# Optimization experiments

Hardware: AMD Instinct MI355X
Metric: run time of the kernel (lower is better)

Reference implementation:

```python
import jax, jax.numpy as jnp
import numpy as np
from jax import lax

HEADS = 8
C, H, W = 64, 16, 16
D_K = C // HEADS
SCALE = 1.0 / np.sqrt(D_K * H * W).astype(np.float32)


def conv2d(x, w, b):
    # x: [N, C, H, W], w: [O, I, 3, 3], padding=1
    y = lax.conv_general_dilated(x, w, window_strides=(1, 1),
                                 padding=((1, 1), (1, 1)),
                                 dimension_numbers=('NCHW', 'OIHW', 'NCHW'))
    return y + b[None, :, None, None]


def _project(x, w, b, bs, seq):
    # x: [bs, seq, C, H, W] -> conv per frame -> [bs, heads, seq, d_k*H*W]
    y = conv2d(x.reshape(bs * seq, C, H, W), w, b)
    y = y.reshape(bs, seq, HEADS, D_K, H, W)
    y = jnp.transpose(y, (0, 2, 1, 3, 4, 5)).reshape(bs, HEADS, seq, D_K * H * W)
    return y


def setup_inputs() -> dict:
    key = jax.random.key(0)
    ks = jax.random.split(key, 11)
    shp = (2, 256, C, H, W)
    wstd = 1.0 / np.sqrt(C * 9)  # torch Conv2d default init scale
    inp = {
        'q': jax.random.normal(ks[0], shp, jnp.float32),
        'k': jax.random.normal(ks[1], shp, jnp.float32),
        'v': jax.random.normal(ks[2], shp, jnp.float32),
        'Wq': jax.random.uniform(ks[3], (C, C, 3, 3), jnp.float32, -wstd, wstd),
        'bq': jax.random.uniform(ks[4], (C,), jnp.float32, -wstd, wstd),
        'Wk': jax.random.uniform(ks[5], (C, C, 3, 3), jnp.float32, -wstd, wstd),
        'bk': jax.random.uniform(ks[6], (C,), jnp.float32, -wstd, wstd),
        'Wv': jax.random.uniform(ks[7], (C, C, 3, 3), jnp.float32, -wstd, wstd),
        'bv': jax.random.uniform(ks[8], (C,), jnp.float32, -wstd, wstd),
        'Wo': jax.random.uniform(ks[9], (C, C, 3, 3), jnp.float32, -wstd, wstd),
        'bo': jax.random.uniform(ks[10], (C,), jnp.float32, -wstd, wstd),
    }
    return inp


def reference(q, k, v, Wq, bq, Wk, bk, Wv, bv, Wo, bo):
    bs, seq = q.shape[0], q.shape[1]
    qh = _project(q, Wq, bq, bs, seq)  # [bs, h, seq, d_k*H*W]
    kh = _project(k, Wk, bk, bs, seq)
    vh = _project(v, Wv, bv, bs, seq)
    scores = jnp.einsum('bhqd,bhkd->bhqk', qh, kh) * SCALE
    attn = jax.nn.softmax(scores, axis=-1)
    out = jnp.einsum('bhqk,bhkd->bhqd', attn, vh)  # [bs, h, seq, d_k*H*W]
    out = out.reshape(bs, HEADS, seq, D_K, H, W)
    concat = jnp.transpose(out, (0, 2, 1, 3, 4, 5)).reshape(bs * seq, C, H, W)
    y = conv2d(concat, Wo, bo).reshape(bs, seq, C, H, W)
    return y
```

## Files before the change

kernel.cpp:

```cpp
#include <hip/hip_runtime.h>
#include <hip/hip_bf16.h>
#include <hip/hip_fp16.h>

typedef unsigned short u16;
typedef _Float16 f16x8 __attribute__((ext_vector_type(8)));
typedef u16 u16x8 __attribute__((ext_vector_type(8)));
typedef u16 u16x4 __attribute__((ext_vector_type(4)));
typedef float f32x4 __attribute__((ext_vector_type(4)));

__device__ __forceinline__ u16 f2h(float f){
  __half h = __float2half(f);
  return *(u16*)&h;
}

__device__ __forceinline__ void cp16_async(const u16* g, u16* l){
  __builtin_amdgcn_global_load_lds(
      (const __attribute__((address_space(1))) unsigned int*)g,
      (__attribute__((address_space(3))) unsigned int*)l,
      16, 0, 0);
}

__device__ __forceinline__ void prep_w_body(const float* W, u16* Wt, int i){
  if (i >= 36864) return;
  int co = i / 576, rem = i % 576, ci = rem / 9, tap = rem % 9;
  int n = co >> 4, lr = co & 15, kk = ci >> 5, lg = (ci >> 3) & 3, j = ci & 7;
  int s = tap*2 + kk;
  Wt[(((s*4 + n)*64) + lg*16 + lr)*8 + j] = f2h(W[i]);
}

__global__ __launch_bounds__(256) void prep_w3(
    const float* __restrict__ Wq, const float* __restrict__ Wk,
    const float* __restrict__ Wv, u16* __restrict__ Wt)
{
  int which = blockIdx.y;
  const float* W = (which == 0) ? Wq : (which == 1) ? Wk : Wv;
  prep_w_body(W, Wt + which*36864, blockIdx.x * 256 + threadIdx.x);
}

__global__ __launch_bounds__(256) void prep_w(
    const float* __restrict__ W, u16* __restrict__ Wt)
{
  prep_w_body(W, Wt, blockIdx.x * 256 + threadIdx.x);
}

template<bool IN_F32, bool OUT_PROJ>
__device__ __forceinline__ void conv_body(
    const void* __restrict__ xin, const u16* __restrict__ Wt,
    const float* __restrict__ bias, void* __restrict__ dst,
    int frame, u16* xT, float* stage, int tid)
{
  #define STAGE_Q(qi, buf) do {                                             \
    if (IN_F32){                                                            \
      const float* src_ = (const float*)xin + (size_t)frame*16384 + (qi)*4096; \
      _Pragma("unroll")                                                     \
      for (int t_ = 0; t_ < 4; ++t_){                                       \
        int c_ = tid + t_*256;                                              \
        cp16_async((const u16*)(src_ + c_*4), (u16*)((float*)(buf) + c_*4));\
      }                                                                     \
    } else {                                                                \
      const u16* src_ = (const u16*)xin + (size_t)frame*16384 + (qi)*4096;  \
      _Pragma("unroll")                                                     \
      for (int t_ = 0; t_ < 2; ++t_){                                       \
        int c_ = tid + t_*256;                                              \
        cp16_async(src_ + c_*8, (u16*)(buf) + c_*8);                        \
      }                                                                     \
    }                                                                       \
  } while(0)

  float* S0 = stage;
  float* S1 = stage + 4096;

  STAGE_Q(0, S0);
  for (int i = tid; i < 2592; i += 256)
    *(uint4*)((char*)xT + i*16) = make_uint4(0u, 0u, 0u, 0u);
  __syncthreads();

  const int p = tid, py = p >> 4, px = p & 15;
  const int pp = (py + 1)*18 + px + 1;

  #pragma unroll 1
  for (int qi = 0; qi < 4; ++qi){
    if (qi < 3) STAGE_Q(qi + 1, (qi & 1) ? S0 : S1);
    const float* Sf = (qi & 1) ? S1 : S0;
    const u16*   Su = (const u16*)Sf;
    #pragma unroll
    for (int b = 0; b < 2; ++b){
      u16x8 pk;
      #pragma unroll
      for (int j = 0; j < 8; ++j)
        pk[j] = IN_F32 ? f2h(Sf[(b*8 + j)*256 + p]) : Su[(b*8 + j)*256 + p];
      unsigned cb = (unsigned)(qi*2 + b);
      unsigned off = (unsigned)(pp*128) + (((cb + (unsigned)pp) & 7u) << 4);
      *(u16x8*)((char*)xT + off) = pk;
    }
    __syncthreads();
  }

  const int w = tid >> 6, lane = tid & 63, lr = lane & 15, lg = lane >> 4;
  const int pyb = w * 4;

  f32x4 acc[4][4];
  #pragma unroll
  for (int n = 0; n < 4; ++n){
    float b = bias[n*16 + lr];
    #pragma unroll
    for (int m = 0; m < 4; ++m){
      acc[m][n][0] = b; acc[m][n][1] = b; acc[m][n][2] = b; acc[m][n][3] = b;
    }
  }

  #define LOADB(s, B) do {                                                  \
    _Pragma("unroll")                                                       \
    for (int n_ = 0; n_ < 4; ++n_)                                          \
      B[n_] = *(const f16x8*)(Wt + ((((s)*4 + n_)*64) + lane)*8);           \
  } while(0)

  #define STEP(s, B) do {                                                   \
    int tap_ = (s) >> 1, kk_ = (s) & 1;                                     \
    int dy_ = tap_ / 3, dx_ = tap_ - dy_*3;                                 \
    f16x8 af_[4];                                                           \
    _Pragma("unroll")                                                       \
    for (int m_ = 0; m_ < 4; ++m_){                                         \
      int pp_ = (pyb + m_ + dy_)*18 + lr + dx_;                             \
      unsigned slot_ = ((unsigned)(kk_*4 + lg) + (unsigned)pp_) & 7u;       \
      af_[m_] = *(const f16x8*)((const char*)xT                             \
                 + (unsigned)(pp_*128) + (slot_ << 4));                     \
    }                                                                       \
    _Pragma("unroll")                                                       \
    for (int m_ = 0; m_ < 4; ++m_)                                          \
      _Pragma("unroll")                                                     \
      for (int n_ = 0; n_ < 4; ++n_)                                        \
        acc[m_][n_] = __builtin_amdgcn_mfma_f32_16x16x32_f16(               \
            af_[m_], B[n_], acc[m_][n_], 0, 0, 0);                          \
  } while(0)

  f16x8 Ba[4], Bb[4];
  LOADB(0, Ba);
  #pragma unroll 1
  for (int it = 0; it < 9; ++it){
    LOADB(it*2 + 1, Bb);
    STEP(it*2, Ba);
    if (it < 8) LOADB(it*2 + 2, Ba);
    STEP(it*2 + 1, Bb);
  }
  #undef LOADB
  #undef STEP
  #undef STAGE_Q

  __syncthreads();
  char* xTc = (char*)xT;
  if (OUT_PROJ){
    #pragma unroll
    for (int n = 0; n < 4; ++n){
      int co = n*16 + lr;
      #pragma unroll
      for (int m = 0; m < 4; ++m){
        int px0 = w*64 + m*16 + lg*4;
        int s = px0 >> 3;
        unsigned aw = (unsigned)(co*512) + (unsigned)((s ^ (co & 7)) << 4)
                      + (unsigned)((px0 & 7) * 2);
        u16x4 o4;
        #pragma unroll
        for (int r = 0; r < 4; ++r) o4[r] = f2h(acc[m][n][r]);
        *(u16x4*)(xTc + aw) = o4;
      }
    }
    __syncthreads();
    u16* d = (u16*)dst;
    const int b = frame >> 8, sq = frame & 255;
    #pragma unroll
    for (int i = 0; i < 8; ++i){
      int c = w*8 + i;
      int co = c*2 + (lane >> 5);
      int pxo = (lane & 31) * 8;
      unsigned ld = (unsigned)(co*512) + (unsigned)(((lane & 31) ^ (co & 7)) << 4);
      uint4 v = *(const uint4*)(xTc + ld);
      int h = co >> 3, dk = co & 7;
      u16* gp = d + ((size_t)((b*8 + h)*256 + sq))*2048 + dk*256 + pxo;
      *(uint4*)gp = v;
    }
  } else {
    float* dfr = (float*)dst + (size_t)frame * 16384;
    #pragma unroll
    for (int ph2 = 0; ph2 < 2; ++ph2){
      if ((w >> 1) == ph2){
        #pragma unroll
        for (int n = 0; n < 4; ++n){
          int co = n*16 + lr;
          #pragma unroll
          for (int m = 0; m < 4; ++m){
            int pxl = (w & 1)*64 + m*16 + lg*4;
            int s = pxl >> 2;
            unsigned aw = (unsigned)(co*512) + (unsigned)((s ^ (co & 7)) << 4);
            *(f32x4*)(xTc + aw) = acc[m][n];
          }
        }
      }
      __syncthreads();
      #pragma unroll
      for (int i = 0; i < 8; ++i){
        int c = w*8 + i;
        int co = c*2 + (lane >> 5);
        int pxl = (lane & 31) * 4;
        unsigned ld = (unsigned)(co*512) + (unsigned)(((lane & 31) ^ (co & 7)) << 4);
        f32x4 v = *(const f32x4*)(xTc + ld);
        *(f32x4*)(dfr + co*256 + ph2*128 + pxl) = v;
      }
      if (ph2 == 0) __syncthreads();
    }
  }
}

__global__ __launch_bounds__(256, 2) void conv3_mfma(
    const float* __restrict__ q, const float* __restrict__ k,
    const float* __restrict__ v, const u16* __restrict__ Wt3,
    const float* __restrict__ bq, const float* __restrict__ bk,
    const float* __restrict__ bv,
    u16* __restrict__ qh, u16* __restrict__ kh, u16* __restrict__ vh)
{
  __shared__ __align__(16) u16 xT[324 * 64];
  __shared__ __align__(16) float stage[2*4096];
  const int which = blockIdx.x >> 9;
  const int frame = blockIdx.x & 511;
  const float* x = (which == 0) ? q : (which == 1) ? k : v;
  const float* bias = (which == 0) ? bq : (which == 1) ? bk : bv;
  u16* dst = (which == 0) ? qh : (which == 1) ? kh : vh;
  conv_body<true, true>(x, Wt3 + which*36864, bias, dst, frame, xT, stage, threadIdx.x);
}

__global__ __launch_bounds__(256, 2) void conv_out_mfma(
    const u16* __restrict__ xin, const u16* __restrict__ Wt,
    const float* __restrict__ bias, float* __restrict__ out)
{
  __shared__ __align__(16) u16 xT[324 * 64];
  __shared__ __align__(16) float stage[2*4096];
  conv_body<false, false>(xin, Wt, bias, out, blockIdx.x, xT, stage, threadIdx.x);
}

__global__ __launch_bounds__(256) void transpose_v(
    const u16* __restrict__ vh, u16* __restrict__ vt)
{
  __shared__ u16 tile[64][72];
  const int tid = threadIdx.x;
  const int dt = blockIdx.x, st = blockIdx.y, bh = blockIdx.z;
  {
    int r = tid >> 2, c4 = tid & 3;
    const u16* src = vh + ((size_t)(bh*256 + st*64 + r))*2048 + dt*64 + c4*16;
    uint4 v0 = *(const uint4*)src;
    uint4 v1 = *(const uint4*)(src + 8);
    *(uint4*)&tile[r][c4*16]     = v0;
    *(uint4*)&tile[r][c4*16 + 8] = v1;
  }
  __syncthreads();
  {
    int dr = tid >> 2, s4 = tid & 3;
    u16 tmp[16];
    #pragma unroll
    for (int i = 0; i < 16; ++i) tmp[i] = tile[s4*16 + i][dr];
    u16* dstp = vt + ((size_t)(bh*2048 + dt*64 + dr))*256 + st*64 + s4*16;
    *(uint4*)dstp       = *(uint4*)&tmp[0];
    *(uint4*)(dstp + 8) = *(uint4*)&tmp[8];
  }
}

__global__ __launch_bounds__(512, 2) void attn_kernel(
    const u16* __restrict__ qh, const u16* __restrict__ kh,
    const u16* __restrict__ vt, u16* __restrict__ obuf)
{
  const float SCALE = 0.022097086912079608f;
  __shared__ __align__(16) u16 Qs[16*2048];
  __shared__ __align__(16) u16 Kb[2][16384];
  __shared__ __align__(16) u16 P[16*256];
  __shared__ float redA[8][16];
  __shared__ float redB[8][16];

  const int tid = threadIdx.x;
  const int w = tid >> 6, lane = tid & 63, lr = lane & 15, lg = lane >> 4;

  const int id = blockIdx.x;
  const int xcd = id & 7, j = id >> 3;
  const int bh = xcd + 8*(j & 1), qt = j >> 1;
  const int q0 = qt * 16, b = bh >> 3, h = bh & 7;

  const u16* Qg = qh + ((size_t)(bh*256 + q0))*2048;
  const u16* Kg = kh + (size_t)bh * 256 * 2048;
  const u16* Vg = vt + (size_t)bh * 2048 * 256;

  const int spK = (lane & 7) ^ ((lane >> 3) & 7);
  #define STAGE_K(c, buf)                                                   \
    _Pragma("unroll")                                                       \
    for (int r_ = 0; r_ < 4; ++r_)                                          \
      cp16_async(Kg + (size_t)(w*32 + r_*8 + (lane>>3))*2048 + (c)*64 + spK*8, \
                 (buf) + w*2048 + r_*512);

  #define STAGE_V(c, buf)                                                   \
    _Pragma("unroll")                                                       \
    for (int r_ = 0; r_ < 8; ++r_){                                         \
      int rl_ = w*16 + r_*2 + (lane>>5);                                    \
      int sp_ = (lane & 31) ^ (rl_ & 7);                                    \
      cp16_async(Vg + (size_t)((c)*128 + rl_)*256 + sp_*8,                  \
                 (buf) + w*4096 + r_*512);                                  \
    }

  #pragma unroll
  for (int r = 0; r < 8; ++r){
    int t = r*64 + lane;
    int row = w*2 + (t >> 8);
    int dp = t & 255;
    int sp = (dp & ~7) | ((dp & 7) ^ (row & 7));
    cp16_async(Qg + (size_t)row*2048 + sp*8, Qs + w*4096 + r*512);
  }
  STAGE_K(0, Kb[0]);
  __syncthreads();

  const f32x4 zero4 = {0.f, 0.f, 0.f, 0.f};
  f32x4 sacc[2] = {zero4, zero4};
  #pragma unroll 1
  for (int c = 0; c < 32; ++c){
    if (c < 31) STAGE_K(c+1, Kb[(c+1)&1]);
    const u16* kb = Kb[c&1];
    #pragma unroll
    for (int d2 = 0; d2 < 2; ++d2){
      unsigned aoff = (((unsigned)lr << 12) + (unsigned)(c*128 + d2*64 + lg*16))
                      ^ (unsigned)((lr & 7) << 4);
      f16x8 a = *(const f16x8*)((const char*)Qs + aoff);
      #pragma unroll
      for (int n = 0; n < 2; ++n){
        int row = w*32 + n*16 + lr;
        const u16* kp = kb + row*64 + (((d2*4 + lg) ^ (row & 7)) << 3);
        f16x8 bk = *(const f16x8*)kp;
        sacc[n] = __builtin_amdgcn_mfma_f32_16x16x32_f16(a, bk, sacc[n], 0,0,0);
      }
    }
    __syncthreads();
  }

  float mx[4];
  #pragma unroll
  for (int r = 0; r < 4; ++r){
    float vv = fmaxf(sacc[0][r], sacc[1][r]);
    #pragma unroll
    for (int off = 1; off < 16; off <<= 1) vv = fmaxf(vv, __shfl_xor(vv, off));
    mx[r] = vv;
  }
  if (lr == 0){
    #pragma unroll
    for (int r = 0; r < 4; ++r) redA[w][lg*4 + r] = mx[r];
  }
  __syncthreads();
  #pragma unroll
  for (int r = 0; r < 4; ++r){
    int row = lg*4 + r;
    float vv = redA[0][row];
    #pragma unroll
    for (int ww = 1; ww < 8; ++ww) vv = fmaxf(vv, redA[ww][row]);
    mx[r] = vv;
  }

  const int kbase = w * 32;
  float sm[4] = {0.f, 0.f, 0.f, 0.f};
  #pragma unroll
  for (int n = 0; n < 2; ++n)
    #pragma unroll
    for (int r = 0; r < 4; ++r){
      float pv = __expf((sacc[n][r] - mx[r]) * SCALE);
      sm[r] += pv;
      int row = lg*4 + r;
      int col = kbase + n*16 + lr;
      unsigned off = (((unsigned)row << 9) + ((unsigned)col << 1))
                     ^ (unsigned)((row & 7) << 4);
      *(u16*)((char*)P + off) = f2h(pv);
    }
  #pragma unroll
  for (int r = 0; r < 4; ++r){
    float vv = sm[r];
    #pragma unroll
    for (int off = 1; off < 16; off <<= 1) vv += __shfl_xor(vv, off);
    sm[r] = vv;
  }
  if (lr == 0){
    #pragma unroll
    for (int r = 0; r < 4; ++r) redB[w][lg*4 + r] = sm[r];
  }
  __syncthreads();
  float rs[4];
  #pragma unroll
  for (int r = 0; r < 4; ++r){
    int row = lg*4 + r;
    float s = redB[0][row];
    #pragma unroll
    for (int ww = 1; ww < 8; ++ww) s += redB[ww][row];
    rs[r] = 1.0f / s;
  }

  u16* Vb0 = Qs;
  u16* Vb1 = &Kb[0][0];
  STAGE_V(0, Vb0);
  __syncthreads();
  #pragma unroll 1
  for (int c = 0; c < 16; ++c){
    if (c < 15){
      u16* nbuf = ((c+1) & 1) ? Vb1 : Vb0;
      STAGE_V(c+1, nbuf);
    }
    const u16* vb = (c & 1) ? Vb1 : Vb0;
    f32x4 oacc = zero4;
    #pragma unroll
    for (int kt = 0; kt < 8; ++kt){
      unsigned poff = (((unsigned)lr << 9) + (unsigned)(kt*64 + lg*16))
                      ^ (unsigned)((lr & 7) << 4);
      f16x8 pa = *(const f16x8*)((const char*)P + poff);
      int row = w*16 + lr;
      const u16* vp = vb + row*256 + (((kt*4 + lg) ^ (row & 7)) << 3);
      f16x8 bv = *(const f16x8*)vp;
      oacc = __builtin_amdgcn_mfma_f32_16x16x32_f16(pa, bv, oacc, 0,0,0);
    }
    #pragma unroll
    for (int r = 0; r < 4; ++r){
      float o = oacc[r] * rs[r];
      int qrow = q0 + lg*4 + r;
      int d = c*128 + w*16 + lr;
      int frame = b*256 + qrow;
      int cdim = h*8 + (d >> 8);
      obuf[((size_t)(frame*64 + cdim))*256 + (d & 255)] = f2h(o);
    }
    __syncthreads();
  }
  #undef STAGE_K
  #undef STAGE_V
}

extern "C" void kernel_launch(void* const* d_in, const int* in_sizes, int n_in,
                              void* d_out, int out_size, void* d_ws, size_t ws_size,
                              hipStream_t stream)
{
  const float* q  = (const float*)d_in[0];
  const float* k  = (const float*)d_in[1];
  const float* v  = (const float*)d_in[2];
  const float* Wq = (const float*)d_in[3];
  const float* bq = (const float*)d_in[4];
  const float* Wk = (const float*)d_in[5];
  const float* bk = (const float*)d_in[6];
  const float* Wv = (const float*)d_in[7];
  const float* bv = (const float*)d_in[8];
  const float* Wo = (const float*)d_in[9];
  const float* bo = (const float*)d_in[10];
  float* out = (float*)d_out;

  char* ws = (char*)d_ws;
  u16* qh = (u16*)(ws);
  u16* kh = (u16*)(ws + (size_t)16*1024*1024);
  u16* vh = (u16*)(ws + (size_t)32*1024*1024);
  u16* vt = (u16*)(ws + (size_t)48*1024*1024);
  u16* obuf = vh;
  u16* Wt3  = vt;
  u16* WtO  = qh;

  prep_w3<<<dim3(144, 3), dim3(256), 0, stream>>>(Wq, Wk, Wv, Wt3);
  conv3_mfma<<<dim3(1536), dim3(256), 0, stream>>>(q, k, v, Wt3, bq, bk, bv,
                                                   qh, kh, vh);
  transpose_v<<<dim3(32, 4, 16), dim3(256), 0, stream>>>(vh, vt);
  attn_kernel<<<dim3(256), dim3(512), 0, stream>>>(qh, kh, vt, obuf);
  prep_w<<<dim3(144), dim3(256), 0, stream>>>(Wo, WtO);
  conv_out_mfma<<<dim3(512), dim3(256), 0, stream>>>(obuf, WtO, bo, out);
}
```

Baseline: 121.7 us.

## Drop LDS staging buffers in conv kernels, load input directly, raise occupancy

The conv kernels no longer stage each input quarter through a double-buffered LDS area with async global-to-LDS copies. Each thread now reads its pixel's 64 channels straight from global memory, converts them and writes the swizzled LDS tile. This removes 32 KB of shared memory per block and the per-quarter barriers, and launch bounds are raised to 3 blocks per CU so more blocks can be resident. The cost is that the overlap of loading and converting is lost, and register pressure may rise under the tighter launch bound.

```diff
diff --git a/kernel.cpp b/kernel.cpp
--- a/kernel.cpp
+++ b/kernel.cpp
@@ -47,54 +47,30 @@
 __device__ __forceinline__ void conv_body(
     const void* __restrict__ xin, const u16* __restrict__ Wt,
     const float* __restrict__ bias, void* __restrict__ dst,
-    int frame, u16* xT, float* stage, int tid)
-{
-  #define STAGE_Q(qi, buf) do {                                             \
-    if (IN_F32){                                                            \
-      const float* src_ = (const float*)xin + (size_t)frame*16384 + (qi)*4096; \
-      _Pragma("unroll")                                                     \
-      for (int t_ = 0; t_ < 4; ++t_){                                       \
-        int c_ = tid + t_*256;                                              \
-        cp16_async((const u16*)(src_ + c_*4), (u16*)((float*)(buf) + c_*4));\
-      }                                                                     \
-    } else {                                                                \
-      const u16* src_ = (const u16*)xin + (size_t)frame*16384 + (qi)*4096;  \
-      _Pragma("unroll")                                                     \
-      for (int t_ = 0; t_ < 2; ++t_){                                       \
-        int c_ = tid + t_*256;                                              \
-        cp16_async(src_ + c_*8, (u16*)(buf) + c_*8);                        \
-      }                                                                     \
-    }                                                                       \
-  } while(0)
-
-  float* S0 = stage;
-  float* S1 = stage + 4096;
-
-  STAGE_Q(0, S0);
+    int frame, u16* xT, int tid)
+{
   for (int i = tid; i < 2592; i += 256)
     *(uint4*)((char*)xT + i*16) = make_uint4(0u, 0u, 0u, 0u);
   __syncthreads();
 
-  const int p = tid, py = p >> 4, px = p & 15;
-  const int pp = (py + 1)*18 + px + 1;
-
-  #pragma unroll 1
-  for (int qi = 0; qi < 4; ++qi){
-    if (qi < 3) STAGE_Q(qi + 1, (qi & 1) ? S0 : S1);
-    const float* Sf = (qi & 1) ? S1 : S0;
-    const u16*   Su = (const u16*)Sf;
-    #pragma unroll
-    for (int b = 0; b < 2; ++b){
+  {
+    const int p = tid, py = p >> 4, px = p & 15;
+    const int pp = (py + 1)*18 + px + 1;
+    const float* xf = (const float*)xin + (size_t)frame * 16384;
+    const u16*   xb = (const u16*)  xin + (size_t)frame * 16384;
+    #pragma unroll
+    for (int cb = 0; cb < 8; ++cb){
       u16x8 pk;
       #pragma unroll
-      for (int j = 0; j < 8; ++j)
-        pk[j] = IN_F32 ? f2h(Sf[(b*8 + j)*256 + p]) : Su[(b*8 + j)*256 + p];
-      unsigned cb = (unsigned)(qi*2 + b);
-      unsigned off = (unsigned)(pp*128) + (((cb + (unsigned)pp) & 7u) << 4);
+      for (int j = 0; j < 8; ++j){
+        int ci = cb*8 + j;
+        pk[j] = IN_F32 ? f2h(xf[ci*256 + p]) : xb[ci*256 + p];
+      }
+      unsigned off = (unsigned)(pp*128) + ((((unsigned)cb + (unsigned)pp) & 7u) << 4);
       *(u16x8*)((char*)xT + off) = pk;
     }
-    __syncthreads();
-  }
+  }
+  __syncthreads();
 
   const int w = tid >> 6, lane = tid & 63, lr = lane & 15, lg = lane >> 4;
   const int pyb = w * 4;
@@ -145,7 +121,6 @@
   }
   #undef LOADB
   #undef STEP
-  #undef STAGE_Q
 
   __syncthreads();
   char* xTc = (char*)xT;
@@ -211,7 +186,7 @@
   }
 }
 
-__global__ __launch_bounds__(256, 2) void conv3_mfma(
+__global__ __launch_bounds__(256, 3) void conv3_mfma(
     const float* __restrict__ q, const float* __restrict__ k,
     const float* __restrict__ v, const u16* __restrict__ Wt3,
     const float* __restrict__ bq, const float* __restrict__ bk,
@@ -219,22 +194,20 @@
     u16* __restrict__ qh, u16* __restrict__ kh, u16* __restrict__ vh)
 {
   __shared__ __align__(16) u16 xT[324 * 64];
-  __shared__ __align__(16) float stage[2*4096];
   const int which = blockIdx.x >> 9;
   const int frame = blockIdx.x & 511;
   const float* x = (which == 0) ? q : (which == 1) ? k : v;
   const float* bias = (which == 0) ? bq : (which == 1) ? bk : bv;
   u16* dst = (which == 0) ? qh : (which == 1) ? kh : vh;
-  conv_body<true, true>(x, Wt3 + which*36864, bias, dst, frame, xT, stage, threadIdx.x);
-}
-
-__global__ __launch_bounds__(256, 2) void conv_out_mfma(
+  conv_body<true, true>(x, Wt3 + which*36864, bias, dst, frame, xT, threadIdx.x);
+}
+
+__global__ __launch_bounds__(256, 3) void conv_out_mfma(
     const u16* __restrict__ xin, const u16* __restrict__ Wt,
     const float* __restrict__ bias, float* __restrict__ out)
 {
   __shared__ __align__(16) u16 xT[324 * 64];
-  __shared__ __align__(16) float stage[2*4096];
-  conv_body<false, false>(xin, Wt, bias, out, blockIdx.x, xT, stage, threadIdx.x);
+  conv_body<false, false>(xin, Wt, bias, out, blockIdx.x, xT, threadIdx.x);
 }
 
 __global__ __launch_bounds__(256) void transpose_v(
```

After: 115.6 us. -5.0%, faster.
